# Kernel tuning notes

Hardware: AMD Instinct MI355X
Metric: run time of the kernel (lower is better)

## Reference

```python
import jax, jax.numpy as jnp
import numpy as np

N = 1024
DIN = 128   # ndim_node_in
P = 64      # ndim_node_out
E = 32      # ndim_edge
H = 2 * P + E  # attention MLP width


def _layer_norm(x, g, b, eps=1e-5):
    m = jnp.mean(x, axis=-1, keepdims=True)
    v = jnp.mean(jnp.square(x - m), axis=-1, keepdims=True)
    return (x - m) * jax.lax.rsqrt(v + eps) * g + b


def setup_inputs() -> dict:
    key = jax.random.key(0)
    ks = jax.random.split(key, 10)
    node_features = jax.random.normal(ks[0], (N, DIN), dtype=jnp.float32)
    edge_features = jax.random.normal(ks[1], (N, N, E), dtype=jnp.float32)
    node_adjacent = jax.random.randint(ks[2], (N, N), 0, 2).astype(jnp.float32)
    s = 0.02
    return {
        "node_features": node_features,
        "edge_features": edge_features,
        "node_adjacent": node_adjacent,
        "ln1_g": jnp.ones((DIN,), jnp.float32),
        "ln1_b": jnp.zeros((DIN,), jnp.float32),
        "W1": jax.random.normal(ks[3], (DIN, P), jnp.float32) * s,
        "b1": jnp.zeros((P,), jnp.float32),
        "Wa1": jax.random.normal(ks[4], (H, H), jnp.float32) * s,
        "ba1": jnp.zeros((H,), jnp.float32),
        "Wa2": jax.random.normal(ks[5], (H, 1), jnp.float32) * s,
        "ba2": jnp.zeros((1,), jnp.float32),
        "ln2_g": jnp.ones((P,), jnp.float32),
        "ln2_b": jnp.zeros((P,), jnp.float32),
    }


def reference(node_features, edge_features, node_adjacent,
              ln1_g, ln1_b, W1, b1, Wa1, ba1, Wa2, ba2, ln2_g, ln2_b):
    # LayerNorm + Linear -> projected node features h [N, P]
    h = _layer_norm(node_features, ln1_g, ln1_b) @ W1 + b1

    # A_norm = D^{-1/2} (A + I) D^{-1/2}
    A = node_adjacent + jnp.eye(node_adjacent.shape[-1], dtype=node_adjacent.dtype)
    d = 1.0 / jnp.sqrt(jnp.sum(A, axis=-1))
    d = jnp.where(jnp.isnan(d), 0.0, d)
    A_norm = d[:, None] * A * d[None, :]

    # Pairwise MLP attention score. Equivalent to concat([h_i, h_j, e_ij]) @ Wa1,
    # computed without materializing the [N, N, 2P] concat by splitting Wa1 rows.
    Wi, Wj, We = Wa1[:P], Wa1[P:2 * P], Wa1[2 * P:]
    hid = (h @ Wi)[:, None, :] + (h @ Wj)[None, :, :] \
        + jnp.einsum('ije,eh->ijh', edge_features, We) + ba1  # [N, N, H]
    hid = jax.nn.gelu(hid, approximate=False)
    score = (hid @ Wa2)[..., 0] + ba2[0]                      # [N, N]

    score = jnp.where(score >= 0, score, 0.2 * score)         # LeakyReLU(0.2)
    score = jnp.where(A_norm > 0, score, jnp.float32(-1e12))  # adjacency mask
    att = jax.nn.softmax(score, axis=-1)

    return _layer_norm(att @ h, ln2_g, ln2_b)
```

## Files before the change

kernel.cpp:

```cpp
#include <hip/hip_runtime.h>
#include <math.h>

#define NN 1024
#define DIN 128
#define PP 64
#define EE 32
#define HH 160

typedef __bf16 bf16x8 __attribute__((ext_vector_type(8)));
typedef float f32x4 __attribute__((ext_vector_type(4)));
typedef _Float16 f16x2 __attribute__((ext_vector_type(2)));

__device__ __forceinline__ float wave_sum(float v) {
#pragma unroll
  for (int o = 32; o > 0; o >>= 1) v += __shfl_xor(v, o);
  return v;
}
__device__ __forceinline__ float wave_max(float v) {
#pragma unroll
  for (int o = 32; o > 0; o >>= 1) v = fmaxf(v, __shfl_xor(v, o));
  return v;
}

__device__ __forceinline__ f16x2 pk2(float a, float b) {
  auto r = __builtin_amdgcn_cvt_pkrtz(a, b);
  return __builtin_bit_cast(f16x2, r);
}

__device__ __forceinline__ f16x2 gelu_pk(f16x2 x) {
  const _Float16 a3 = (_Float16)(-5.92240e-4f);
  const _Float16 a2 = (_Float16)(8.94359e-3f);
  const _Float16 a1 = (_Float16)(-6.607936e-2f);
  const _Float16 a0 = (_Float16)(0.39894228f);
  const _Float16 hl = (_Float16)(0.5f);
  f16x2 t = x * x;
  f16x2 g = ((a3 * t + a2) * t + a1) * t + a0;
  f16x2 ph = x * g + hl;
  return x * ph;
}

__device__ __forceinline__ float h2add_bits(float a, float b) {
  f16x2 r = __builtin_bit_cast(f16x2, a) + __builtin_bit_cast(f16x2, b);
  return __builtin_bit_cast(float, r);
}

__global__ __launch_bounds__(256) void setup_kernel(
    const float* __restrict__ x,
    const float* __restrict__ g1, const float* __restrict__ b1ln,
    const float* __restrict__ W1, const float* __restrict__ b1,
    const float* __restrict__ Wa1, const float* __restrict__ ba1,
    const float* __restrict__ adj,
    __bf16* __restrict__ hbf_out, float* __restrict__ hib_out,
    __bf16* __restrict__ Bpack,
    unsigned short* __restrict__ jidx, int* __restrict__ cnt)
{
  const int b = blockIdx.x;
  const int t = threadIdx.x;

  if (b < NN) {
    const int i = b;
    const int wv = t >> 6, lane = t & 63;
    __shared__ int wt[4];
    unsigned long long m[4];
    int tot = 0;
#pragma unroll
    for (int r = 0; r < 4; ++r) {
      int j = wv * 256 + r * 64 + lane;
      bool flag = (adj[(size_t)i * NN + j] > 0.f) || (j == i);
      m[r] = __ballot(flag);
      tot += (int)__popcll(m[r]);
    }
    if (lane == 0) wt[wv] = tot;
    __syncthreads();
    int off = 0;
    for (int w = 0; w < wv; ++w) off += wt[w];
    const unsigned long long lt = (1ull << lane) - 1ull;
#pragma unroll
    for (int r = 0; r < 4; ++r) {
      if ((m[r] >> lane) & 1ull) {
        int pos = off + (int)__popcll(m[r] & lt);
        jidx[(size_t)i * NN + pos] = (unsigned short)(wv * 256 + r * 64 + lane);
      }
      off += (int)__popcll(m[r]);
    }
    if (t == 0) cnt[i] = wt[0] + wt[1] + wt[2] + wt[3];
  } else if (b == NN) {
    for (int idx = t; idx < 15360; idx += 256) {
      int e  = idx & 7;
      int c  = (idx >> 3) & 15;
      int rg = (idx >> 7) & 3;
      int fc = idx >> 9;
      int f = fc / 3, chunk = fc - 3 * f;
      int k = chunk * 32 + rg * 8 + e;
      int grow = (k < 32) ? (2 * PP + k) : (PP + (k - 32));
      Bpack[idx] = (__bf16)Wa1[(size_t)grow * HH + f * 16 + c];
    }
  } else {
    const int i = b - NN - 1;
    __shared__ float xraw[DIN];
    __shared__ float xn[DIN];
    __shared__ float hrow[PP];
    __shared__ float red[2];
    if (t < DIN) xraw[t] = x[(size_t)i * DIN + t];
    __syncthreads();
    if (t < 64) {
      float a = xraw[t], bb = xraw[t + 64];
      float s  = wave_sum(a + bb);
      float sq = wave_sum(a * a + bb * bb);
      if (t == 0) {
        float mm = s * (1.f / DIN);
        float v = sq * (1.f / DIN) - mm * mm;
        red[0] = mm;
        red[1] = rsqrtf(v + 1e-5f);
      }
    }
    __syncthreads();
    if (t < DIN) xn[t] = (xraw[t] - red[0]) * red[1] * g1[t] + b1ln[t];
    __syncthreads();
    if (t < PP) {
      float acc = b1[t];
#pragma unroll 8
      for (int k = 0; k < DIN; ++k) acc += xn[k] * W1[(size_t)k * PP + t];
      hrow[t] = acc;
      hbf_out[(size_t)i * PP + t] = (__bf16)acc;
    }
    __syncthreads();
    if (t < HH) {
      float a1 = ba1[t];
#pragma unroll 8
      for (int p = 0; p < PP; ++p) a1 += hrow[p] * Wa1[(size_t)p * HH + t];
      hib_out[(size_t)i * HH + t] = a1;
    }
  }
}

__global__ __launch_bounds__(512, 4) void scores_kernel(
    const float* __restrict__ edge,
    const __bf16* __restrict__ Bpack_g, const float* __restrict__ Wa2,
    const float* __restrict__ ba2,
    const float* __restrict__ hib, const __bf16* __restrict__ hbf,
    const unsigned short* __restrict__ jidx, const int* __restrict__ cnt_g,
    _Float16* __restrict__ scbuf)
{
  const int b = blockIdx.x;
  const int i = b >> 1;
  const int half = b & 1;
  const int cnt = cnt_g[i];
  const int h0 = (cnt + 1) >> 1;
  const int base   = half ? h0 : 0;
  const int n_here = half ? (cnt - h0) : h0;
  if (n_here <= 0) return;

  const int t = threadIdx.x;
  const int wave = t >> 6;
  const int lane = t & 63;
  const int c  = lane & 15;
  const int rg = lane >> 4;

  __shared__ float4 BpV[1920];
  __shared__ unsigned int hibw2_s[HH];
  __shared__ unsigned short jidx_s[512];
  const __bf16* Bp = (const __bf16*)BpV;

  {
    const float4* src = (const float4*)Bpack_g;
    for (int idx = t; idx < 1920; idx += 512) BpV[idx] = src[idx];
  }
  for (int idx = t; idx < n_here; idx += 512)
    jidx_s[idx] = jidx[(size_t)i * NN + base + idx];
  if (t < HH)
    hibw2_s[t] = __builtin_bit_cast(unsigned int,
                                    pk2(hib[(size_t)i * HH + t], Wa2[t]));
  const float ba2v = ba2[0];
  __syncthreads();

  const float* eb0 = edge + (size_t)i * NN * EE + rg * 8;
  const int nt = (n_here + 15) >> 4;

  for (int tt = wave; tt < nt; tt += 8) {
    int pc = tt * 16 + c;
    if (pc > n_here - 1) pc = n_here - 1;
    const int jj = jidx_s[pc];

    float4 ea = *(const float4*)(eb0 + (size_t)jj * EE);
    float4 eb = *(const float4*)(eb0 + (size_t)jj * EE + 4);
    bf16x8 a1 = *(const bf16x8*)(hbf + (size_t)jj * PP + rg * 8);
    bf16x8 a2 = *(const bf16x8*)(hbf + (size_t)jj * PP + rg * 8 + 32);
    bf16x8 a0;
    a0[0] = (__bf16)ea.x; a0[1] = (__bf16)ea.y;
    a0[2] = (__bf16)ea.z; a0[3] = (__bf16)ea.w;
    a0[4] = (__bf16)eb.x; a0[5] = (__bf16)eb.y;
    a0[6] = (__bf16)eb.z; a0[7] = (__bf16)eb.w;

    f16x2 sc01 = {(_Float16)0.f, (_Float16)0.f};
    f16x2 sc23 = {(_Float16)0.f, (_Float16)0.f};
#pragma unroll 2
    for (int f = 0; f < 10; ++f) {
      const __bf16* bbase = Bp + f * 1536 + rg * 128 + c * 8;
      f32x4 acc = {0.f, 0.f, 0.f, 0.f};
      acc = __builtin_amdgcn_mfma_f32_16x16x32_bf16(
          a0, *(const bf16x8*)(bbase), acc, 0, 0, 0);
      acc = __builtin_amdgcn_mfma_f32_16x16x32_bf16(
          a1, *(const bf16x8*)(bbase + 512), acc, 0, 0, 0);
      acc = __builtin_amdgcn_mfma_f32_16x16x32_bf16(
          a2, *(const bf16x8*)(bbase + 1024), acc, 0, 0, 0);

      f16x2 hw = __builtin_bit_cast(f16x2, hibw2_s[f * 16 + c]);
      f16x2 base2; base2[0] = hw[0]; base2[1] = hw[0];
      f16x2 w2p;   w2p[0]   = hw[1]; w2p[1]   = hw[1];
      f16x2 x01 = pk2(acc[0], acc[1]) + base2;
      f16x2 x23 = pk2(acc[2], acc[3]) + base2;
      sc01 = gelu_pk(x01) * w2p + sc01;
      sc23 = gelu_pk(x23) * w2p + sc23;
    }
    float v01 = __builtin_bit_cast(float, sc01);
    float v23 = __builtin_bit_cast(float, sc23);
#pragma unroll
    for (int m = 1; m <= 8; m <<= 1) {
      v01 = h2add_bits(v01, __shfl_xor(v01, m));
      v23 = h2add_bits(v23, __shfl_xor(v23, m));
    }
    if (c == 0) {
      f16x2 r01 = __builtin_bit_cast(f16x2, v01);
      f16x2 r23 = __builtin_bit_cast(f16x2, v23);
      float sf[4] = {(float)r01[0], (float)r01[1],
                     (float)r23[0], (float)r23[1]};
#pragma unroll
      for (int r = 0; r < 4; ++r) {
        const int pos = tt * 16 + rg * 4 + r;
        if (pos < n_here) {
          float s = sf[r] + ba2v;
          s = (s >= 0.f) ? s : 0.2f * s;
          scbuf[(size_t)i * NN + base + pos] = (_Float16)s;
        }
      }
    }
  }
}

__global__ __launch_bounds__(256) void finish_kernel(
    const _Float16* __restrict__ scbuf,
    const float* __restrict__ g2, const float* __restrict__ b2,
    const __bf16* __restrict__ hbf,
    const unsigned short* __restrict__ jidx, const int* __restrict__ cnt_g,
    float* __restrict__ out)
{
  const int i = blockIdx.x;
  const int t = threadIdx.x;
  const int wave = t >> 6;
  const int lane = t & 63;

  __shared__ float sc_s[NN];
  __shared__ unsigned short jidx_s[NN];
  __shared__ float red_s[8];
  __shared__ float obuf[4][PP];

  const int cnt = cnt_g[i];
  if (t < 128)
    ((uint4*)jidx_s)[t] = ((const uint4*)(jidx + (size_t)i * NN))[t];
  for (int p_ = t; p_ < cnt; p_ += 256)
    sc_s[p_] = (float)scbuf[(size_t)i * NN + p_];
  __syncthreads();

  float mx = -INFINITY;
  for (int p_ = t; p_ < cnt; p_ += 256) mx = fmaxf(mx, sc_s[p_]);
  mx = wave_max(mx);
  if (lane == 0) red_s[wave] = mx;
  __syncthreads();
  mx = fmaxf(fmaxf(red_s[0], red_s[1]), fmaxf(red_s[2], red_s[3]));
  float ps = 0.f;
  for (int p_ = t; p_ < cnt; p_ += 256) {
    float e_ = __expf(sc_s[p_] - mx);
    sc_s[p_] = e_;
    ps += e_;
  }
  ps = wave_sum(ps);
  if (lane == 0) red_s[4 + wave] = ps;
  __syncthreads();
  const float inv = 1.f / (red_s[4] + red_s[5] + red_s[6] + red_s[7]);
  __syncthreads();

  {
    const int p = t & 63;
    const int g = t >> 6;
    float ac0 = 0.f, ac1 = 0.f, ac2 = 0.f, ac3 = 0.f;
    int pos = g;
    for (; pos + 12 < cnt; pos += 16) {
      int j0 = jidx_s[pos];
      int j1 = jidx_s[pos + 4];
      int j2 = jidx_s[pos + 8];
      int j3 = jidx_s[pos + 12];
      float v0 = (float)hbf[(size_t)j0 * PP + p];
      float v1 = (float)hbf[(size_t)j1 * PP + p];
      float v2 = (float)hbf[(size_t)j2 * PP + p];
      float v3 = (float)hbf[(size_t)j3 * PP + p];
      ac0 = fmaf(sc_s[pos],      v0, ac0);
      ac1 = fmaf(sc_s[pos + 4],  v1, ac1);
      ac2 = fmaf(sc_s[pos + 8],  v2, ac2);
      ac3 = fmaf(sc_s[pos + 12], v3, ac3);
    }
    for (; pos < cnt; pos += 4)
      ac0 = fmaf(sc_s[pos], (float)hbf[(size_t)jidx_s[pos] * PP + p], ac0);
    obuf[g][p] = (ac0 + ac1) + (ac2 + ac3);
  }
  __syncthreads();
  if (t < PP) {
    float v = (obuf[0][t] + obuf[1][t] + obuf[2][t] + obuf[3][t]) * inv;
    float s = wave_sum(v);
    float mean = s * (1.f / PP);
    float d = v - mean;
    float var = wave_sum(d * d) * (1.f / PP);
    out[(size_t)i * PP + t] = d * rsqrtf(var + 1e-5f) * g2[t] + b2[t];
  }
}

extern "C" void kernel_launch(void* const* d_in, const int* in_sizes, int n_in,
                              void* d_out, int out_size, void* d_ws, size_t ws_size,
                              hipStream_t stream) {
  const float* node_features = (const float*)d_in[0];
  const float* edge_features = (const float*)d_in[1];
  const float* node_adjacent = (const float*)d_in[2];
  const float* ln1_g = (const float*)d_in[3];
  const float* ln1_b = (const float*)d_in[4];
  const float* W1    = (const float*)d_in[5];
  const float* b1    = (const float*)d_in[6];
  const float* Wa1   = (const float*)d_in[7];
  const float* ba1   = (const float*)d_in[8];
  const float* Wa2   = (const float*)d_in[9];
  const float* ba2   = (const float*)d_in[10];
  const float* ln2_g = (const float*)d_in[11];
  const float* ln2_b = (const float*)d_in[12];
  float* out = (float*)d_out;

  char* ws = (char*)d_ws;
  float*  hib_ws   = (float*)(ws);
  __bf16* Bpack_ws = (__bf16*)(ws + 655360);
  __bf16* hbf_ws   = (__bf16*)(ws + 686080);
  unsigned short* jidx_ws = (unsigned short*)(ws + 817152);
  int*    cnt_ws   = (int*)(ws + 2914304);
  _Float16* scbuf_ws = (_Float16*)(ws + 2918400);

  setup_kernel<<<2 * NN + 1, 256, 0, stream>>>(
      node_features, ln1_g, ln1_b, W1, b1, Wa1, ba1, node_adjacent,
      hbf_ws, hib_ws, Bpack_ws, jidx_ws, cnt_ws);
  scores_kernel<<<2 * NN, 512, 0, stream>>>(
      edge_features, Bpack_ws, Wa2, ba2, hib_ws, hbf_ws, jidx_ws, cnt_ws,
      scbuf_ws);
  finish_kernel<<<NN, 256, 0, stream>>>(
      scbuf_ws, ln2_g, ln2_b, hbf_ws, jidx_ws, cnt_ws, out);
}
```

Measured before the change: 60.68 us.

## Fuse score computation with softmax and aggregation into one per-row kernel

After: 56.36 us, median of 3. 7.1% less time.

```diff
diff --git a/kernel.cpp b/kernel.cpp
--- a/kernel.cpp
+++ b/kernel.cpp
@@ -134,23 +134,16 @@
   }
 }
 
-__global__ __launch_bounds__(512, 4) void scores_kernel(
+__global__ __launch_bounds__(512, 4) void gat_main_kernel(
     const float* __restrict__ edge,
     const __bf16* __restrict__ Bpack_g, const float* __restrict__ Wa2,
-    const float* __restrict__ ba2,
+    const float* __restrict__ ba2, const float* __restrict__ g2,
+    const float* __restrict__ b2,
     const float* __restrict__ hib, const __bf16* __restrict__ hbf,
     const unsigned short* __restrict__ jidx, const int* __restrict__ cnt_g,
-    _Float16* __restrict__ scbuf)
+    float* __restrict__ out)
 {
-  const int b = blockIdx.x;
-  const int i = b >> 1;
-  const int half = b & 1;
-  const int cnt = cnt_g[i];
-  const int h0 = (cnt + 1) >> 1;
-  const int base   = half ? h0 : 0;
-  const int n_here = half ? (cnt - h0) : h0;
-  if (n_here <= 0) return;
-
+  const int i = blockIdx.x;
   const int t = threadIdx.x;
   const int wave = t >> 6;
   const int lane = t & 63;
@@ -158,16 +151,20 @@
   const int rg = lane >> 4;
 
   __shared__ float4 BpV[1920];
+  __shared__ float sc_s[NN];
+  __shared__ unsigned short jidx_s[NN];
   __shared__ unsigned int hibw2_s[HH];
-  __shared__ unsigned short jidx_s[512];
+  __shared__ float red_s[16];
+  __shared__ float obuf[8][PP];
   const __bf16* Bp = (const __bf16*)BpV;
 
+  const int cnt = cnt_g[i];
   {
     const float4* src = (const float4*)Bpack_g;
     for (int idx = t; idx < 1920; idx += 512) BpV[idx] = src[idx];
   }
-  for (int idx = t; idx < n_here; idx += 512)
-    jidx_s[idx] = jidx[(size_t)i * NN + base + idx];
+  if (t < 128)
+    ((uint4*)jidx_s)[t] = ((const uint4*)(jidx + (size_t)i * NN))[t];
   if (t < HH)
     hibw2_s[t] = __builtin_bit_cast(unsigned int,
                                     pk2(hib[(size_t)i * HH + t], Wa2[t]));
@@ -175,11 +172,11 @@
   __syncthreads();
 
   const float* eb0 = edge + (size_t)i * NN * EE + rg * 8;
-  const int nt = (n_here + 15) >> 4;
+  const int nt = (cnt + 15) >> 4;
 
   for (int tt = wave; tt < nt; tt += 8) {
     int pc = tt * 16 + c;
-    if (pc > n_here - 1) pc = n_here - 1;
+    if (pc > cnt - 1) pc = cnt - 1;
     const int jj = jidx_s[pc];
 
     float4 ea = *(const float4*)(eb0 + (size_t)jj * EE);
@@ -228,84 +225,56 @@
 #pragma unroll
       for (int r = 0; r < 4; ++r) {
         const int pos = tt * 16 + rg * 4 + r;
-        if (pos < n_here) {
+        if (pos < cnt) {
           float s = sf[r] + ba2v;
-          s = (s >= 0.f) ? s : 0.2f * s;
-          scbuf[(size_t)i * NN + base + pos] = (_Float16)s;
+          sc_s[pos] = (s >= 0.f) ? s : 0.2f * s;
         }
       }
     }
   }
-}
-
-__global__ __launch_bounds__(256) void finish_kernel(
-    const _Float16* __restrict__ scbuf,
-    const float* __restrict__ g2, const float* __restrict__ b2,
-    const __bf16* __restrict__ hbf,
-    const unsigned short* __restrict__ jidx, const int* __restrict__ cnt_g,
-    float* __restrict__ out)
-{
-  const int i = blockIdx.x;
-  const int t = threadIdx.x;
-  const int wave = t >> 6;
-  const int lane = t & 63;
-
-  __shared__ float sc_s[NN];
-  __shared__ unsigned short jidx_s[NN];
-  __shared__ float red_s[8];
-  __shared__ float obuf[4][PP];
-
-  const int cnt = cnt_g[i];
-  if (t < 128)
-    ((uint4*)jidx_s)[t] = ((const uint4*)(jidx + (size_t)i * NN))[t];
-  for (int p_ = t; p_ < cnt; p_ += 256)
-    sc_s[p_] = (float)scbuf[(size_t)i * NN + p_];
   __syncthreads();
 
   float mx = -INFINITY;
-  for (int p_ = t; p_ < cnt; p_ += 256) mx = fmaxf(mx, sc_s[p_]);
+  for (int p_ = t; p_ < cnt; p_ += 512) mx = fmaxf(mx, sc_s[p_]);
   mx = wave_max(mx);
   if (lane == 0) red_s[wave] = mx;
   __syncthreads();
-  mx = fmaxf(fmaxf(red_s[0], red_s[1]), fmaxf(red_s[2], red_s[3]));
+  mx = fmaxf(fmaxf(fmaxf(red_s[0], red_s[1]), fmaxf(red_s[2], red_s[3])),
+             fmaxf(fmaxf(red_s[4], red_s[5]), fmaxf(red_s[6], red_s[7])));
   float ps = 0.f;
-  for (int p_ = t; p_ < cnt; p_ += 256) {
+  for (int p_ = t; p_ < cnt; p_ += 512) {
     float e_ = __expf(sc_s[p_] - mx);
     sc_s[p_] = e_;
     ps += e_;
   }
   ps = wave_sum(ps);
-  if (lane == 0) red_s[4 + wave] = ps;
-  __syncthreads();
-  const float inv = 1.f / (red_s[4] + red_s[5] + red_s[6] + red_s[7]);
+  if (lane == 0) red_s[8 + wave] = ps;
+  __syncthreads();
+  const float inv = 1.f / (((red_s[8] + red_s[9]) + (red_s[10] + red_s[11])) +
+                           ((red_s[12] + red_s[13]) + (red_s[14] + red_s[15])));
   __syncthreads();
 
   {
     const int p = t & 63;
     const int g = t >> 6;
-    float ac0 = 0.f, ac1 = 0.f, ac2 = 0.f, ac3 = 0.f;
+    float ac0 = 0.f, ac1 = 0.f;
     int pos = g;
-    for (; pos + 12 < cnt; pos += 16) {
+    for (; pos + 8 < cnt; pos += 16) {
       int j0 = jidx_s[pos];
-      int j1 = jidx_s[pos + 4];
-      int j2 = jidx_s[pos + 8];
-      int j3 = jidx_s[pos + 12];
+      int j1 = jidx_s[pos + 8];
       float v0 = (float)hbf[(size_t)j0 * PP + p];
       float v1 = (float)hbf[(size_t)j1 * PP + p];
-      float v2 = (float)hbf[(size_t)j2 * PP + p];
-      float v3 = (float)hbf[(size_t)j3 * PP + p];
-      ac0 = fmaf(sc_s[pos],      v0, ac0);
-      ac1 = fmaf(sc_s[pos + 4],  v1, ac1);
-      ac2 = fmaf(sc_s[pos + 8],  v2, ac2);
-      ac3 = fmaf(sc_s[pos + 12], v3, ac3);
-    }
-    for (; pos < cnt; pos += 4)
+      ac0 = fmaf(sc_s[pos],     v0, ac0);
+      ac1 = fmaf(sc_s[pos + 8], v1, ac1);
+    }
+    for (; pos < cnt; pos += 8)
       ac0 = fmaf(sc_s[pos], (float)hbf[(size_t)jidx_s[pos] * PP + p], ac0);
-    obuf[g][p] = (ac0 + ac1) + (ac2 + ac3);
+    obuf[g][p] = ac0 + ac1;
   }
   __syncthreads();
   if (t < PP) {
-    float v = (obuf[0][t] + obuf[1][t] + obuf[2][t] + obuf[3][t]) * inv;
+    float v = (((obuf[0][t] + obuf[1][t]) + (obuf[2][t] + obuf[3][t])) +
+               ((obuf[4][t] + obuf[5][t]) + (obuf[6][t] + obuf[7][t]))) * inv;
     float s = wave_sum(v);
     float mean = s * (1.f / PP);
     float d = v - mean;
@@ -338,14 +307,11 @@
   __bf16* hbf_ws   = (__bf16*)(ws + 686080);
   unsigned short* jidx_ws = (unsigned short*)(ws + 817152);
   int*    cnt_ws   = (int*)(ws + 2914304);
-  _Float16* scbuf_ws = (_Float16*)(ws + 2918400);
 
   setup_kernel<<<2 * NN + 1, 256, 0, stream>>>(
       node_features, ln1_g, ln1_b, W1, b1, Wa1, ba1, node_adjacent,
       hbf_ws, hib_ws, Bpack_ws, jidx_ws, cnt_ws);
-  scores_kernel<<<2 * NN, 512, 0, stream>>>(
-      edge_features, Bpack_ws, Wa2, ba2, hib_ws, hbf_ws, jidx_ws, cnt_ws,
-      scbuf_ws);
-  finish_kernel<<<NN, 256, 0, stream>>>(
-      scbuf_ws, ln2_g, ln2_b, hbf_ws, jidx_ws, cnt_ws, out);
-}
+  gat_main_kernel<<<NN, 512, 0, stream>>>(
+      edge_features, Bpack_ws, Wa2, ba2, ln2_g, ln2_b, hib_ws, hbf_ws,
+      jidx_ws, cnt_ws, out);
+}
```
